# Kernel optimization log

Measured on AMD Instinct MI355X. Metric: run time of the kernel, lower is better.

## Reference

```python
import jax, jax.numpy as jnp
import numpy as np

TOP_K = 3
THRESH = 0.2
# scales=[1] -> multi_scale_fft reduces to one full-length window:
# combined_amplitudes = |rfft(x, axis=1)|.mean(channels)

def setup_inputs() -> dict:
    key = jax.random.key(0)
    x = jax.random.normal(key, (64, 4096, 64), dtype=jnp.float32)
    return {"x": x}

def _autocorr_score(xi, p):
    # xi: [T, C]; p: scalar int32 period (guaranteed in [2, T//2]).
    # Equivalent to mean over consecutive period-segments i of
    # cosine_similarity(flatten(seg_i), flatten(seg_{i+1})) — computed via
    # prefix sums of lag-p cross products so the segment reshape never needs
    # a data-dependent shape.
    T, C = xi.shape
    t = jnp.arange(T)
    tp = t + p
    m = (tp < T).astype(xi.dtype)
    xs = xi[jnp.clip(tp, 0, T - 1)]                  # [T, C] rows shifted by p
    r = (xi * xs).sum(-1) * m                        # <x[t], x[t+p]>
    q = (xi * xi).sum(-1)                            # ||x[t]||^2
    z = jnp.zeros((1,), xi.dtype)
    CR = jnp.concatenate([z, jnp.cumsum(r)])         # [T+1]
    CQ = jnp.concatenate([z, jnp.cumsum(q)])
    nper = T // p
    i = jnp.arange(T // 2)                           # max possible segments (p>=2)
    seg = i < (nper - 1)
    s = jnp.clip(i * p, 0, T)
    e = jnp.clip((i + 1) * p, 0, T)
    e2 = jnp.clip((i + 2) * p, 0, T)
    dots = CR[e] - CR[s]                             # flat dot(seg_i, seg_{i+1})
    na = jnp.sqrt(jnp.maximum(CQ[e] - CQ[s], 0.0))
    nb = jnp.sqrt(jnp.maximum(CQ[e2] - CQ[e], 0.0))
    cos = dots / jnp.maximum(na * nb, 1e-8)          # F.cosine_similarity eps
    denom = jnp.maximum(nper - 1, 1).astype(xi.dtype)
    score = jnp.where(seg, cos, 0.0).sum() / denom
    return jnp.where(nper >= 2, score, 0.0)

def reference(x):
    B, T, C = x.shape
    half = T // 2
    # multi-scale FFT with scales=[1]: single window == full sequence
    amps = jnp.abs(jnp.fft.rfft(x, axis=1)).mean(-1)       # [B, T//2+1]
    _, idx = jax.lax.top_k(amps, 2 * TOP_K)                 # [B, 2K]
    period_f = T / (idx + 1).astype(jnp.float32)            # candidate periods
    in_range = (period_f >= 2.0) & (period_f <= half)       # float-period filter
    p_int = jnp.clip(jnp.floor(period_f).astype(jnp.int32), 2, half)
    pf_floor = jnp.floor(period_f)
    in_range_int = (pf_floor >= 2.0) & (pf_floor <= half)   # int-period filter
    # autocorrelation validation score per (batch, candidate)
    scores = jax.vmap(lambda xi, ps: jax.vmap(lambda p: _autocorr_score(xi, p))(ps))(x, p_int)  # [B, 2K]
    valid = in_range & in_range_int & (scores > THRESH)
    # deterministic fallback periods (torch.randint branch unreachable for TOP_K=3)
    common = np.array([T // 4, T // 3, T // 2, int(T / 1.5)], dtype=np.int32)
    common = common[(common >= 2) & (common <= half)]
    add = jnp.asarray(common)                               # [>= TOP_K]

    def select(p_row, v_row):
        order = jnp.argsort(jnp.logical_not(v_row), stable=True)  # valid first, order kept
        sp = p_row[order][:TOP_K]
        cnt = jnp.minimum(v_row.sum(), TOP_K)
        j = jnp.arange(TOP_K)
        filled = jnp.where(j < cnt, sp, add[jnp.clip(j - cnt, 0, add.shape[0] - 1)])
        w = jnp.where(j < cnt, 1.0, 0.5)
        return filled.astype(jnp.float32), w.astype(jnp.float32)

    periods, weights = jax.vmap(select)(p_int, valid)       # [B, TOP_K] each
    return periods, weights
```

## Files before the change

kernel.cpp:

```cpp
#include <hip/hip_runtime.h>
#include <math.h>

#define T_LEN 4096
#define C_CH 64
#define B_N 64
#define NBINS 2049
#define K2 6
#define TOPK 3
#define THRESH_V 0.2f

#define PIDX(i) ((i) + ((i) >> 5))
#define ZSZ (T_LEN + (T_LEN >> 5))

__device__ __forceinline__ unsigned short f2bf(float v) {
    unsigned int u = __float_as_uint(v);
    u += 0x7FFFu + ((u >> 16) & 1u);
    return (unsigned short)(u >> 16);
}
__device__ __forceinline__ float bf2f(unsigned short h) {
    return __uint_as_float(((unsigned int)h) << 16);
}

__device__ __forceinline__ float2 cmul(float2 a, float2 b) {
    return make_float2(a.x * b.x - a.y * b.y, a.x * b.y + a.y * b.x);
}
__device__ __forceinline__ float2 cadd(float2 a, float2 b) { return make_float2(a.x + b.x, a.y + b.y); }
__device__ __forceinline__ float2 csub(float2 a, float2 b) { return make_float2(a.x - b.x, a.y - b.y); }

__device__ __forceinline__ void dft16(float2* v) {
    const float C2 = 0.70710678118654752f;
    const float C1 = 0.92387953251128676f;
    const float S1 = 0.38268343236508977f;
    const int br[16] = {0, 8, 4, 12, 2, 10, 6, 14, 1, 9, 5, 13, 3, 11, 7, 15};
    float2 a[16];
#pragma unroll
    for (int i = 0; i < 16; ++i) a[i] = v[br[i]];
#pragma unroll
    for (int g = 0; g < 16; g += 2) {
        float2 t = a[g + 1];
        a[g + 1] = csub(a[g], t);
        a[g] = cadd(a[g], t);
    }
#pragma unroll
    for (int g = 0; g < 16; g += 4) {
        {
            float2 t = a[g + 2];
            a[g + 2] = csub(a[g], t);
            a[g] = cadd(a[g], t);
        }
        {
            float2 t = make_float2(a[g + 3].y, -a[g + 3].x);
            a[g + 3] = csub(a[g + 1], t);
            a[g + 1] = cadd(a[g + 1], t);
        }
    }
    {
        const float2 W4[4] = {{1.f, 0.f}, {C2, -C2}, {0.f, -1.f}, {-C2, -C2}};
#pragma unroll
        for (int g = 0; g < 16; g += 8)
#pragma unroll
            for (int j = 0; j < 4; ++j) {
                float2 t = cmul(W4[j], a[g + 4 + j]);
                a[g + 4 + j] = csub(a[g + j], t);
                a[g + j] = cadd(a[g + j], t);
            }
    }
    {
        const float2 W8[8] = {{1.f, 0.f}, {C1, -S1}, {C2, -C2}, {S1, -C1},
                              {0.f, -1.f}, {-S1, -C1}, {-C2, -C2}, {-C1, -S1}};
#pragma unroll
        for (int j = 0; j < 8; ++j) {
            float2 t = cmul(W8[j], a[8 + j]);
            a[8 + j] = csub(a[j], t);
            a[j] = cadd(a[j], t);
        }
    }
#pragma unroll
    for (int i = 0; i < 16; ++i) v[i] = a[i];
}

__global__ void transpose_cvt_kernel(const float* __restrict__ x,
                                     unsigned short* __restrict__ xtbf) {
    __shared__ float tile[64][65];
    const int b = blockIdx.y;
    const int t0 = blockIdx.x * 64;
    const int lane = threadIdx.x & 63;
    const int w = threadIdx.x >> 6;
    const float* xb = x + (size_t)b * T_LEN * C_CH;
#pragma unroll
    for (int i = 0; i < 16; ++i) {
        int r = w * 16 + i;
        tile[r][lane] = xb[(size_t)(t0 + r) * C_CH + lane];
    }
    __syncthreads();
    const int half = lane >> 5;
    const int tc = (lane & 31) * 2;
#pragma unroll
    for (int it = 0; it < 8; ++it) {
        int c = it * 8 + w * 2 + half;
        float v0 = tile[tc][c];
        float v1 = tile[tc + 1][c];
        unsigned int o = (unsigned int)f2bf(v0) | ((unsigned int)f2bf(v1) << 16);
        unsigned int* dst = (unsigned int*)(xtbf + ((size_t)b * C_CH + c) * T_LEN + t0);
        dst[lane & 31] = o;
    }
}

template <int MODE>
__global__ void fft_amp_kernel(const void* __restrict__ srcv, float* __restrict__ amps) {
    __shared__ float2 Z[ZSZ];
    const int pair = blockIdx.x;
    const int b = blockIdx.y;
    const int tid = threadIdx.x;

    if (MODE == 0) {
        const unsigned short* r0 =
            (const unsigned short*)srcv + ((size_t)b * C_CH + pair * 2) * T_LEN;
        const unsigned short* r1 = r0 + T_LEN;
#pragma unroll
        for (int k = 0; k < 2; ++k) {
            int t0 = k * 2048 + tid * 8;
            uint4 u0 = *(const uint4*)(r0 + t0);
            uint4 u1 = *(const uint4*)(r1 + t0);
            unsigned int a[4] = {u0.x, u0.y, u0.z, u0.w};
            unsigned int c[4] = {u1.x, u1.y, u1.z, u1.w};
#pragma unroll
            for (int j = 0; j < 4; ++j) {
                Z[PIDX(t0 + 2 * j)] = make_float2(__uint_as_float(a[j] << 16),
                                                  __uint_as_float(c[j] << 16));
                Z[PIDX(t0 + 2 * j + 1)] = make_float2(__uint_as_float(a[j] & 0xFFFF0000u),
                                                      __uint_as_float(c[j] & 0xFFFF0000u));
            }
        }
    } else {
        const float* x = (const float*)srcv;
        const int c0 = pair * 2;
        for (int t = tid; t < T_LEN; t += 256)
            Z[PIDX(t)] = *(const float2*)(x + ((size_t)b * T_LEN + t) * C_CH + c0);
    }
    __syncthreads();

    {
        float2 v[16];
#pragma unroll
        for (int t = 0; t < 16; ++t) v[t] = Z[PIDX(tid + 256 * t)];
        dft16(v);
        float s, c;
        __sincosf(-(float)tid * 1.5339807878856412e-3f, &s, &c);
        float2 w1 = make_float2(c, s), w = w1;
#pragma unroll
        for (int r = 1; r < 16; ++r) {
            v[r] = cmul(v[r], w);
            w = cmul(w, w1);
        }
#pragma unroll
        for (int r = 0; r < 16; ++r) Z[PIDX(256 * r + tid)] = v[r];
    }
    __syncthreads();

    {
        const int r = tid >> 4, mu = tid & 15;
        float2 v[16];
#pragma unroll
        for (int nu = 0; nu < 16; ++nu) v[nu] = Z[PIDX(256 * r + mu + 16 * nu)];
        dft16(v);
        float s, c;
        __sincosf(-(float)mu * 2.4543692606170259e-2f, &s, &c);
        float2 w1 = make_float2(c, s), w = w1;
#pragma unroll
        for (int rho = 1; rho < 16; ++rho) {
            v[rho] = cmul(v[rho], w);
            w = cmul(w, w1);
        }
#pragma unroll
        for (int rho = 0; rho < 16; ++rho) Z[PIDX(256 * r + mu + 16 * rho)] = v[rho];
    }
    __builtin_amdgcn_wave_barrier();

    {
        const int r = tid >> 4, rho = tid & 15;
        float2 v[16];
#pragma unroll
        for (int mu = 0; mu < 16; ++mu) v[mu] = Z[PIDX(256 * r + mu + 16 * rho)];
        dft16(v);
#pragma unroll
        for (int mp = 0; mp < 16; ++mp) Z[PIDX(256 * r + mp + 16 * rho)] = v[mp];
    }
    __syncthreads();

    for (int k = tid; k < NBINS; k += 256) {
        int km = (T_LEN - k) & (T_LEN - 1);
        int sk = 256 * (k & 15) + 16 * ((k >> 4) & 15) + (k >> 8);
        int sm = 256 * (km & 15) + 16 * ((km >> 4) & 15) + (km >> 8);
        float2 zk = Z[PIDX(sk)];
        float2 zm = Z[PIDX(sm)];
        float ax = 0.5f * (zk.x + zm.x);
        float ay = 0.5f * (zk.y - zm.y);
        float bx = 0.5f * (zk.y + zm.y);
        float by = -0.5f * (zk.x - zm.x);
        float amp = sqrtf(ax * ax + ay * ay) + sqrtf(bx * bx + by * by);
        atomicAdd(&amps[(size_t)b * NBINS + k], amp);
    }
}

__global__ void topk_kernel(const float* __restrict__ amps, int* __restrict__ p_int,
                            int* __restrict__ preval) {
    __shared__ float vals[NBINS];
    __shared__ float sval[256];
    __shared__ int sidx[256];
    __shared__ int sel[K2];
    const int b = blockIdx.x;
    const int tid = threadIdx.x;
    for (int k = tid; k < NBINS; k += 256) vals[k] = amps[(size_t)b * NBINS + k];
    __syncthreads();
    for (int pass = 0; pass < K2; ++pass) {
        float bv = -INFINITY;
        int bi = NBINS;
        for (int k = tid; k < NBINS; k += 256) {
            float v = vals[k];
            if (v > bv || (v == bv && k < bi)) { bv = v; bi = k; }
        }
        sval[tid] = bv;
        sidx[tid] = bi;
        __syncthreads();
        for (int off = 128; off > 0; off >>= 1) {
            if (tid < off) {
                float ov = sval[tid + off];
                int oi = sidx[tid + off];
                if (ov > sval[tid] || (ov == sval[tid] && oi < sidx[tid])) {
                    sval[tid] = ov;
                    sidx[tid] = oi;
                }
            }
            __syncthreads();
        }
        if (tid == 0) {
            sel[pass] = sidx[0];
            vals[sidx[0]] = -INFINITY;
        }
        __syncthreads();
    }
    if (tid < K2) {
        int idx = sel[tid];
        float pf = (float)T_LEN / (float)(idx + 1);
        int ir = (pf >= 2.0f) && (pf <= (float)(T_LEN / 2));
        float pff = floorf(pf);
        int iri = (pff >= 2.0f) && (pff <= (float)(T_LEN / 2));
        int pi = (int)pff;
        pi = pi < 2 ? 2 : (pi > T_LEN / 2 ? T_LEN / 2 : pi);
        p_int[b * K2 + tid] = pi;
        preval[b * K2 + tid] = ir && iri;
    }
}

__global__ void rq_kernel(const unsigned short* __restrict__ xtbf,
                          const int* __restrict__ p_int, float* __restrict__ r_ws,
                          float* __restrict__ q_ws) {
    const int b = blockIdx.y;
    const int t = blockIdx.x * 64 + threadIdx.x;
    const unsigned short* xb = xtbf + (size_t)b * C_CH * T_LEN;

    int tpc[K2];
    float m[K2];
#pragma unroll
    for (int j = 0; j < K2; ++j) {
        int tp = t + p_int[b * K2 + j];
        m[j] = (tp < T_LEN) ? 1.f : 0.f;
        tpc[j] = (tp < T_LEN) ? tp : (T_LEN - 1);
    }

    float qacc = 0.f;
    float racc[K2] = {0.f, 0.f, 0.f, 0.f, 0.f, 0.f};
    for (int cc = 0; cc < C_CH; cc += 8) {
        float a[8];
        float bv[K2][8];
#pragma unroll
        for (int k = 0; k < 8; ++k) a[k] = bf2f(xb[(size_t)(cc + k) * T_LEN + t]);
#pragma unroll
        for (int j = 0; j < K2; ++j)
#pragma unroll
            for (int k = 0; k < 8; ++k)
                bv[j][k] = bf2f(xb[(size_t)(cc + k) * T_LEN + tpc[j]]);
#pragma unroll
        for (int k = 0; k < 8; ++k) {
            qacc += a[k] * a[k];
#pragma unroll
            for (int j = 0; j < K2; ++j) racc[j] += a[k] * bv[j][k];
        }
    }
    q_ws[(size_t)b * T_LEN + t] = qacc;
#pragma unroll
    for (int j = 0; j < K2; ++j)
        r_ws[((size_t)b * K2 + j) * T_LEN + t] = racc[j] * m[j];
}

__device__ __forceinline__ void block_scan_4096(float* a, float* tsum, int tid) {
    float loc[16];
    const int base = tid * 16;
    float s = 0.f;
#pragma unroll
    for (int i = 0; i < 16; ++i) {
        s += a[base + i];
        loc[i] = s;
    }
    tsum[tid] = s;
    __syncthreads();
    for (int off = 1; off < 256; off <<= 1) {
        float v = (tid >= off) ? tsum[tid - off] : 0.f;
        __syncthreads();
        tsum[tid] += v;
        __syncthreads();
    }
    float offs = tsum[tid] - s;
#pragma unroll
    for (int i = 0; i < 16; ++i) a[base + i] = offs + loc[i];
    __syncthreads();
}

__device__ __forceinline__ void do_select(int b, const int* p_int, const int* preval,
                                          const float* scores, float* out) {
    int sel[TOPK];
    int cnt = 0;
    for (int j = 0; j < K2; ++j) {
        if (preval[b * K2 + j] && scores[b * K2 + j] > THRESH_V) {
            if (cnt < TOPK) sel[cnt] = p_int[b * K2 + j];
            cnt++;
        }
    }
    if (cnt > TOPK) cnt = TOPK;
    int add[4];
    int nadd = 0;
    int cms[4] = {T_LEN / 4, T_LEN / 3, T_LEN / 2, (int)((float)T_LEN / 1.5f)};
    for (int i = 0; i < 4; ++i)
        if (cms[i] >= 2 && cms[i] <= T_LEN / 2) add[nadd++] = cms[i];
    for (int j = 0; j < TOPK; ++j) {
        float pv, wv;
        if (j < cnt) {
            pv = (float)sel[j];
            wv = 1.0f;
        } else {
            int a = j - cnt;
            if (a > nadd - 1) a = nadd - 1;
            pv = (float)add[a];
            wv = 0.5f;
        }
        out[b * TOPK + j] = pv;
        out[B_N * TOPK + b * TOPK + j] = wv;
    }
}

__global__ void score_kernel(const float* __restrict__ r_ws, const float* __restrict__ q_ws,
                             const int* __restrict__ p_int, const int* __restrict__ preval,
                             float* __restrict__ scores, int* __restrict__ counter,
                             float* __restrict__ out) {
    __shared__ float r_s[T_LEN];
    __shared__ float q_s[T_LEN];
    __shared__ float tsum[256];
    __shared__ int lastflag;
    const int cand = blockIdx.x;
    const int b = blockIdx.y;
    const int tid = threadIdx.x;
    const int p = p_int[b * K2 + cand];
    const float4* rsrc = (const float4*)(r_ws + ((size_t)b * K2 + cand) * T_LEN);
    const float4* qsrc = (const float4*)(q_ws + (size_t)b * T_LEN);
    for (int i = tid; i < T_LEN / 4; i += 256) {
        ((float4*)r_s)[i] = rsrc[i];
        ((float4*)q_s)[i] = qsrc[i];
    }
    __syncthreads();
    block_scan_4096(r_s, tsum, tid);
    block_scan_4096(q_s, tsum, tid);
    const int nper = T_LEN / p;
    float part = 0.f;
    for (int i = tid; i < nper - 1; i += 256) {
        int s0 = i * p;
        int e = s0 + p;
        int e2 = e + p;
        float crs = s0 ? r_s[s0 - 1] : 0.f;
        float dots = r_s[e - 1] - crs;
        float cqs = s0 ? q_s[s0 - 1] : 0.f;
        float qa = q_s[e - 1] - cqs;
        float qb = q_s[e2 - 1] - q_s[e - 1];
        float na = sqrtf(fmaxf(qa, 0.f));
        float nb = sqrtf(fmaxf(qb, 0.f));
        part += dots / fmaxf(na * nb, 1e-8f);
    }
    tsum[tid] = part;
    __syncthreads();
    for (int off = 128; off > 0; off >>= 1) {
        if (tid < off) tsum[tid] += tsum[tid + off];
        __syncthreads();
    }
    if (tid == 0) {
        scores[b * K2 + cand] = tsum[0] / (float)(nper - 1);
        __threadfence();
        int old = atomicAdd(counter, 1);
        lastflag = (old == K2 * B_N - 1) ? 1 : 0;
    }
    __syncthreads();
    if (lastflag && tid < B_N) {
        __threadfence();
        do_select(tid, p_int, preval, scores, out);
    }
}

__global__ void autocorr_kernel(const float* __restrict__ x, const int* __restrict__ p_int,
                                float* __restrict__ scores) {
    __shared__ float r_s[T_LEN];
    __shared__ float q_s[T_LEN];
    __shared__ float tsum[256];
    const int cand = blockIdx.x;
    const int b = blockIdx.y;
    const int tid = threadIdx.x;
    const int p = p_int[b * K2 + cand];
    const float* xb = x + (size_t)b * T_LEN * C_CH;
    for (int t = tid; t < T_LEN; t += 256) {
        const float4* row = (const float4*)(xb + (size_t)t * C_CH);
        float q = 0.f, r = 0.f;
        if (t + p < T_LEN) {
            const float4* row2 = (const float4*)(xb + (size_t)(t + p) * C_CH);
#pragma unroll
            for (int i = 0; i < 16; ++i) {
                float4 a = row[i], c = row2[i];
                r += a.x * c.x + a.y * c.y + a.z * c.z + a.w * c.w;
                q += a.x * a.x + a.y * a.y + a.z * a.z + a.w * a.w;
            }
        } else {
#pragma unroll
            for (int i = 0; i < 16; ++i) {
                float4 a = row[i];
                q += a.x * a.x + a.y * a.y + a.z * a.z + a.w * a.w;
            }
        }
        r_s[t] = r;
        q_s[t] = q;
    }
    __syncthreads();
    block_scan_4096(r_s, tsum, tid);
    block_scan_4096(q_s, tsum, tid);
    const int nper = T_LEN / p;
    float part = 0.f;
    for (int i = tid; i < nper - 1; i += 256) {
        int s0 = i * p;
        int e = s0 + p;
        int e2 = e + p;
        float crs = s0 ? r_s[s0 - 1] : 0.f;
        float dots = r_s[e - 1] - crs;
        float cqs = s0 ? q_s[s0 - 1] : 0.f;
        float qa = q_s[e - 1] - cqs;
        float qb = q_s[e2 - 1] - q_s[e - 1];
        float na = sqrtf(fmaxf(qa, 0.f));
        float nb = sqrtf(fmaxf(qb, 0.f));
        part += dots / fmaxf(na * nb, 1e-8f);
    }
    tsum[tid] = part;
    __syncthreads();
    for (int off = 128; off > 0; off >>= 1) {
        if (tid < off) tsum[tid] += tsum[tid + off];
        __syncthreads();
    }
    if (tid == 0) scores[b * K2 + cand] = tsum[0] / (float)(nper - 1);
}

__global__ void select_kernel(const int* __restrict__ p_int, const int* __restrict__ preval,
                              const float* __restrict__ scores, float* __restrict__ out) {
    const int b = threadIdx.x;
    if (b >= B_N) return;
    do_select(b, p_int, preval, scores, out);
}

static size_t align256(size_t v) { return (v + 255) & ~(size_t)255; }

extern "C" void kernel_launch(void* const* d_in, const int* in_sizes, int n_in,
                              void* d_out, int out_size, void* d_ws, size_t ws_size,
                              hipStream_t stream) {
    const float* x = (const float*)d_in[0];
    float* out = (float*)d_out;
    char* ws = (char*)d_ws;

    const size_t amps_b = align256((size_t)B_N * NBINS * sizeof(float));
    const size_t int_b = align256((size_t)B_N * K2 * sizeof(int));
    const size_t r_b = align256((size_t)B_N * K2 * T_LEN * sizeof(float));
    const size_t q_b = align256((size_t)B_N * T_LEN * sizeof(float));
    const size_t xtbf_b = align256((size_t)B_N * T_LEN * C_CH * sizeof(short));

    size_t off = 0;
    float* amps = (float*)(ws + off); off += amps_b;
    int* p_int = (int*)(ws + off); off += int_b;
    int* preval = (int*)(ws + off); off += int_b;
    float* scores = (float*)(ws + off); off += int_b;
    int* counter = (int*)(ws + off); off += 256;
    float* r_ws = (float*)(ws + off); off += r_b;
    float* q_ws = (float*)(ws + off); off += q_b;
    unsigned short* xtbf = (unsigned short*)(ws + off); off += xtbf_b;
    const size_t full_need = off;

    hipMemsetAsync(amps, 0, amps_b, stream);
    hipMemsetAsync(counter, 0, sizeof(int), stream);

    if (ws_size >= full_need) {
        transpose_cvt_kernel<<<dim3(T_LEN / 64, B_N), 256, 0, stream>>>(x, xtbf);
        fft_amp_kernel<0><<<dim3(C_CH / 2, B_N), 256, 0, stream>>>(xtbf, amps);
        topk_kernel<<<B_N, 256, 0, stream>>>(amps, p_int, preval);
        rq_kernel<<<dim3(T_LEN / 64, B_N), 64, 0, stream>>>(xtbf, p_int, r_ws, q_ws);
        score_kernel<<<dim3(K2, B_N), 256, 0, stream>>>(r_ws, q_ws, p_int, preval, scores,
                                                        counter, out);
    } else {
        fft_amp_kernel<1><<<dim3(C_CH / 2, B_N), 256, 0, stream>>>(x, amps);
        topk_kernel<<<B_N, 256, 0, stream>>>(amps, p_int, preval);
        autocorr_kernel<<<dim3(K2, B_N), 256, 0, stream>>>(x, p_int, scores);
        select_kernel<<<1, 64, 0, stream>>>(p_int, preval, scores, out);
    }
}
```

Before: 177.3 us.

## Fuse top-k into FFT kernel via last-block reduction, drop memsets and atomics

```diff
diff --git a/kernel.cpp b/kernel.cpp
--- a/kernel.cpp
+++ b/kernel.cpp
@@ -5,6 +5,7 @@
 #define C_CH 64
 #define B_N 64
 #define NBINS 2049
+#define APITCH 2052
 #define K2 6
 #define TOPK 3
 #define THRESH_V 0.2f
@@ -79,140 +80,8 @@
     for (int i = 0; i < 16; ++i) v[i] = a[i];
 }
 
-__global__ void transpose_cvt_kernel(const float* __restrict__ x,
-                                     unsigned short* __restrict__ xtbf) {
-    __shared__ float tile[64][65];
-    const int b = blockIdx.y;
-    const int t0 = blockIdx.x * 64;
-    const int lane = threadIdx.x & 63;
-    const int w = threadIdx.x >> 6;
-    const float* xb = x + (size_t)b * T_LEN * C_CH;
-#pragma unroll
-    for (int i = 0; i < 16; ++i) {
-        int r = w * 16 + i;
-        tile[r][lane] = xb[(size_t)(t0 + r) * C_CH + lane];
-    }
-    __syncthreads();
-    const int half = lane >> 5;
-    const int tc = (lane & 31) * 2;
-#pragma unroll
-    for (int it = 0; it < 8; ++it) {
-        int c = it * 8 + w * 2 + half;
-        float v0 = tile[tc][c];
-        float v1 = tile[tc + 1][c];
-        unsigned int o = (unsigned int)f2bf(v0) | ((unsigned int)f2bf(v1) << 16);
-        unsigned int* dst = (unsigned int*)(xtbf + ((size_t)b * C_CH + c) * T_LEN + t0);
-        dst[lane & 31] = o;
-    }
-}
-
-template <int MODE>
-__global__ void fft_amp_kernel(const void* __restrict__ srcv, float* __restrict__ amps) {
-    __shared__ float2 Z[ZSZ];
-    const int pair = blockIdx.x;
-    const int b = blockIdx.y;
-    const int tid = threadIdx.x;
-
-    if (MODE == 0) {
-        const unsigned short* r0 =
-            (const unsigned short*)srcv + ((size_t)b * C_CH + pair * 2) * T_LEN;
-        const unsigned short* r1 = r0 + T_LEN;
-#pragma unroll
-        for (int k = 0; k < 2; ++k) {
-            int t0 = k * 2048 + tid * 8;
-            uint4 u0 = *(const uint4*)(r0 + t0);
-            uint4 u1 = *(const uint4*)(r1 + t0);
-            unsigned int a[4] = {u0.x, u0.y, u0.z, u0.w};
-            unsigned int c[4] = {u1.x, u1.y, u1.z, u1.w};
-#pragma unroll
-            for (int j = 0; j < 4; ++j) {
-                Z[PIDX(t0 + 2 * j)] = make_float2(__uint_as_float(a[j] << 16),
-                                                  __uint_as_float(c[j] << 16));
-                Z[PIDX(t0 + 2 * j + 1)] = make_float2(__uint_as_float(a[j] & 0xFFFF0000u),
-                                                      __uint_as_float(c[j] & 0xFFFF0000u));
-            }
-        }
-    } else {
-        const float* x = (const float*)srcv;
-        const int c0 = pair * 2;
-        for (int t = tid; t < T_LEN; t += 256)
-            Z[PIDX(t)] = *(const float2*)(x + ((size_t)b * T_LEN + t) * C_CH + c0);
-    }
-    __syncthreads();
-
-    {
-        float2 v[16];
-#pragma unroll
-        for (int t = 0; t < 16; ++t) v[t] = Z[PIDX(tid + 256 * t)];
-        dft16(v);
-        float s, c;
-        __sincosf(-(float)tid * 1.5339807878856412e-3f, &s, &c);
-        float2 w1 = make_float2(c, s), w = w1;
-#pragma unroll
-        for (int r = 1; r < 16; ++r) {
-            v[r] = cmul(v[r], w);
-            w = cmul(w, w1);
-        }
-#pragma unroll
-        for (int r = 0; r < 16; ++r) Z[PIDX(256 * r + tid)] = v[r];
-    }
-    __syncthreads();
-
-    {
-        const int r = tid >> 4, mu = tid & 15;
-        float2 v[16];
-#pragma unroll
-        for (int nu = 0; nu < 16; ++nu) v[nu] = Z[PIDX(256 * r + mu + 16 * nu)];
-        dft16(v);
-        float s, c;
-        __sincosf(-(float)mu * 2.4543692606170259e-2f, &s, &c);
-        float2 w1 = make_float2(c, s), w = w1;
-#pragma unroll
-        for (int rho = 1; rho < 16; ++rho) {
-            v[rho] = cmul(v[rho], w);
-            w = cmul(w, w1);
-        }
-#pragma unroll
-        for (int rho = 0; rho < 16; ++rho) Z[PIDX(256 * r + mu + 16 * rho)] = v[rho];
-    }
-    __builtin_amdgcn_wave_barrier();
-
-    {
-        const int r = tid >> 4, rho = tid & 15;
-        float2 v[16];
-#pragma unroll
-        for (int mu = 0; mu < 16; ++mu) v[mu] = Z[PIDX(256 * r + mu + 16 * rho)];
-        dft16(v);
-#pragma unroll
-        for (int mp = 0; mp < 16; ++mp) Z[PIDX(256 * r + mp + 16 * rho)] = v[mp];
-    }
-    __syncthreads();
-
-    for (int k = tid; k < NBINS; k += 256) {
-        int km = (T_LEN - k) & (T_LEN - 1);
-        int sk = 256 * (k & 15) + 16 * ((k >> 4) & 15) + (k >> 8);
-        int sm = 256 * (km & 15) + 16 * ((km >> 4) & 15) + (km >> 8);
-        float2 zk = Z[PIDX(sk)];
-        float2 zm = Z[PIDX(sm)];
-        float ax = 0.5f * (zk.x + zm.x);
-        float ay = 0.5f * (zk.y - zm.y);
-        float bx = 0.5f * (zk.y + zm.y);
-        float by = -0.5f * (zk.x - zm.x);
-        float amp = sqrtf(ax * ax + ay * ay) + sqrtf(bx * bx + by * by);
-        atomicAdd(&amps[(size_t)b * NBINS + k], amp);
-    }
-}
-
-__global__ void topk_kernel(const float* __restrict__ amps, int* __restrict__ p_int,
-                            int* __restrict__ preval) {
-    __shared__ float vals[NBINS];
-    __shared__ float sval[256];
-    __shared__ int sidx[256];
-    __shared__ int sel[K2];
-    const int b = blockIdx.x;
-    const int tid = threadIdx.x;
-    for (int k = tid; k < NBINS; k += 256) vals[k] = amps[(size_t)b * NBINS + k];
-    __syncthreads();
+__device__ __forceinline__ void topk_select(float* vals, float* sval, int* sidx, int* sel,
+                                            int b, int tid, int* p_int, int* preval) {
     for (int pass = 0; pass < K2; ++pass) {
         float bv = -INFINITY;
         int bi = NBINS;
@@ -251,6 +120,174 @@
         p_int[b * K2 + tid] = pi;
         preval[b * K2 + tid] = ir && iri;
     }
+}
+
+__global__ void transpose_cvt_kernel(const float* __restrict__ x,
+                                     unsigned short* __restrict__ xtbf,
+                                     int* __restrict__ cnts) {
+    __shared__ float tile[64][65];
+    const int b = blockIdx.y;
+    const int t0 = blockIdx.x * 64;
+    const int lane = threadIdx.x & 63;
+    const int w = threadIdx.x >> 6;
+    if (blockIdx.x == 0 && blockIdx.y == 0 && threadIdx.x < B_N + 1)
+        cnts[threadIdx.x] = 0;
+    const float* xb = x + (size_t)b * T_LEN * C_CH;
+#pragma unroll
+    for (int i = 0; i < 16; ++i) {
+        int r = w * 16 + i;
+        tile[r][lane] = xb[(size_t)(t0 + r) * C_CH + lane];
+    }
+    __syncthreads();
+    const int half = lane >> 5;
+    const int tc = (lane & 31) * 2;
+#pragma unroll
+    for (int it = 0; it < 8; ++it) {
+        int c = it * 8 + w * 2 + half;
+        float v0 = tile[tc][c];
+        float v1 = tile[tc + 1][c];
+        unsigned int o = (unsigned int)f2bf(v0) | ((unsigned int)f2bf(v1) << 16);
+        unsigned int* dst = (unsigned int*)(xtbf + ((size_t)b * C_CH + c) * T_LEN + t0);
+        dst[lane & 31] = o;
+    }
+}
+
+template <int MODE>
+__global__ void fft_amp_kernel(const void* __restrict__ srcv, float* __restrict__ apart,
+                               int* __restrict__ cnts, int* __restrict__ p_int,
+                               int* __restrict__ preval) {
+    __shared__ float2 Z[ZSZ];
+    __shared__ int lastflag;
+    const int pair = blockIdx.x;
+    const int b = blockIdx.y;
+    const int tid = threadIdx.x;
+
+    if (MODE == 0) {
+        const unsigned short* r0 =
+            (const unsigned short*)srcv + ((size_t)b * C_CH + pair * 2) * T_LEN;
+        const unsigned short* r1 = r0 + T_LEN;
+#pragma unroll
+        for (int k = 0; k < 2; ++k) {
+            int t0 = k * 2048 + tid * 8;
+            uint4 u0 = *(const uint4*)(r0 + t0);
+            uint4 u1 = *(const uint4*)(r1 + t0);
+            unsigned int a[4] = {u0.x, u0.y, u0.z, u0.w};
+            unsigned int c[4] = {u1.x, u1.y, u1.z, u1.w};
+#pragma unroll
+            for (int j = 0; j < 4; ++j) {
+                Z[PIDX(t0 + 2 * j)] = make_float2(__uint_as_float(a[j] << 16),
+                                                  __uint_as_float(c[j] << 16));
+                Z[PIDX(t0 + 2 * j + 1)] = make_float2(__uint_as_float(a[j] & 0xFFFF0000u),
+                                                      __uint_as_float(c[j] & 0xFFFF0000u));
+            }
+        }
+    } else {
+        const float* x = (const float*)srcv;
+        const int c0 = pair * 2;
+        for (int t = tid; t < T_LEN; t += 256)
+            Z[PIDX(t)] = *(const float2*)(x + ((size_t)b * T_LEN + t) * C_CH + c0);
+    }
+    __syncthreads();
+
+    {
+        float2 v[16];
+#pragma unroll
+        for (int t = 0; t < 16; ++t) v[t] = Z[PIDX(tid + 256 * t)];
+        dft16(v);
+        float s, c;
+        __sincosf(-(float)tid * 1.5339807878856412e-3f, &s, &c);
+        float2 w1 = make_float2(c, s), w = w1;
+#pragma unroll
+        for (int r = 1; r < 16; ++r) {
+            v[r] = cmul(v[r], w);
+            w = cmul(w, w1);
+        }
+#pragma unroll
+        for (int r = 0; r < 16; ++r) Z[PIDX(256 * r + tid)] = v[r];
+    }
+    __syncthreads();
+
+    {
+        const int r = tid >> 4, mu = tid & 15;
+        float2 v[16];
+#pragma unroll
+        for (int nu = 0; nu < 16; ++nu) v[nu] = Z[PIDX(256 * r + mu + 16 * nu)];
+        dft16(v);
+        float s, c;
+        __sincosf(-(float)mu * 2.4543692606170259e-2f, &s, &c);
+        float2 w1 = make_float2(c, s), w = w1;
+#pragma unroll
+        for (int rho = 1; rho < 16; ++rho) {
+            v[rho] = cmul(v[rho], w);
+            w = cmul(w, w1);
+        }
+#pragma unroll
+        for (int rho = 0; rho < 16; ++rho) Z[PIDX(256 * r + mu + 16 * rho)] = v[rho];
+    }
+    __builtin_amdgcn_wave_barrier();
+
+    {
+        const int r = tid >> 4, rho = tid & 15;
+        float2 v[16];
+#pragma unroll
+        for (int mu = 0; mu < 16; ++mu) v[mu] = Z[PIDX(256 * r + mu + 16 * rho)];
+        dft16(v);
+#pragma unroll
+        for (int mp = 0; mp < 16; ++mp) Z[PIDX(256 * r + mp + 16 * rho)] = v[mp];
+    }
+    __syncthreads();
+
+    float* mypart = apart + ((size_t)b * 32 + pair) * APITCH;
+    for (int k = tid; k < NBINS; k += 256) {
+        int km = (T_LEN - k) & (T_LEN - 1);
+        int sk = 256 * (k & 15) + 16 * ((k >> 4) & 15) + (k >> 8);
+        int sm = 256 * (km & 15) + 16 * ((km >> 4) & 15) + (km >> 8);
+        float2 zk = Z[PIDX(sk)];
+        float2 zm = Z[PIDX(sm)];
+        float ax = 0.5f * (zk.x + zm.x);
+        float ay = 0.5f * (zk.y - zm.y);
+        float bx = 0.5f * (zk.y + zm.y);
+        float by = -0.5f * (zk.x - zm.x);
+        float amp = sqrtf(ax * ax + ay * ay) + sqrtf(bx * bx + by * by);
+        if (MODE == 0)
+            mypart[k] = amp;
+        else
+            atomicAdd(&apart[(size_t)b * NBINS + k], amp);
+    }
+
+    if (MODE != 0) return;
+
+    __threadfence();
+    if (tid == 0) lastflag = (atomicAdd(&cnts[b], 1) == 31) ? 1 : 0;
+    __syncthreads();
+    if (!lastflag) return;
+    __threadfence();
+
+    float* vals = (float*)Z;
+    float* sval = vals + NBINS;
+    int* sidx = (int*)(sval + 256);
+    int* sel = sidx + 256;
+    const float* bp = apart + (size_t)b * 32 * APITCH;
+    for (int k = tid; k < NBINS; k += 256) {
+        float s = 0.f;
+        for (int p2 = 0; p2 < 32; ++p2) s += bp[(size_t)p2 * APITCH + k];
+        vals[k] = s;
+    }
+    __syncthreads();
+    topk_select(vals, sval, sidx, sel, b, tid, p_int, preval);
+}
+
+__global__ void topk_kernel(const float* __restrict__ amps, int* __restrict__ p_int,
+                            int* __restrict__ preval) {
+    __shared__ float vals[NBINS];
+    __shared__ float sval[256];
+    __shared__ int sidx[256];
+    __shared__ int sel[K2];
+    const int b = blockIdx.x;
+    const int tid = threadIdx.x;
+    for (int k = tid; k < NBINS; k += 256) vals[k] = amps[(size_t)b * NBINS + k];
+    __syncthreads();
+    topk_select(vals, sval, sidx, sel, b, tid, p_int, preval);
 }
 
 __global__ void rq_kernel(const unsigned short* __restrict__ xtbf,
@@ -478,36 +515,34 @@
     float* out = (float*)d_out;
     char* ws = (char*)d_ws;
 
-    const size_t amps_b = align256((size_t)B_N * NBINS * sizeof(float));
+    const size_t cnt_b = 256;
     const size_t int_b = align256((size_t)B_N * K2 * sizeof(int));
+    const size_t apart_b = align256((size_t)B_N * 32 * APITCH * sizeof(float));
     const size_t r_b = align256((size_t)B_N * K2 * T_LEN * sizeof(float));
     const size_t q_b = align256((size_t)B_N * T_LEN * sizeof(float));
     const size_t xtbf_b = align256((size_t)B_N * T_LEN * C_CH * sizeof(short));
 
     size_t off = 0;
-    float* amps = (float*)(ws + off); off += amps_b;
+    int* cnts = (int*)(ws + off); off += cnt_b;
     int* p_int = (int*)(ws + off); off += int_b;
     int* preval = (int*)(ws + off); off += int_b;
     float* scores = (float*)(ws + off); off += int_b;
-    int* counter = (int*)(ws + off); off += 256;
+    float* apart = (float*)(ws + off); off += apart_b;
     float* r_ws = (float*)(ws + off); off += r_b;
     float* q_ws = (float*)(ws + off); off += q_b;
     unsigned short* xtbf = (unsigned short*)(ws + off); off += xtbf_b;
     const size_t full_need = off;
 
-    hipMemsetAsync(amps, 0, amps_b, stream);
-    hipMemsetAsync(counter, 0, sizeof(int), stream);
-
     if (ws_size >= full_need) {
-        transpose_cvt_kernel<<<dim3(T_LEN / 64, B_N), 256, 0, stream>>>(x, xtbf);
-        fft_amp_kernel<0><<<dim3(C_CH / 2, B_N), 256, 0, stream>>>(xtbf, amps);
-        topk_kernel<<<B_N, 256, 0, stream>>>(amps, p_int, preval);
+        transpose_cvt_kernel<<<dim3(T_LEN / 64, B_N), 256, 0, stream>>>(x, xtbf, cnts);
+        fft_amp_kernel<0><<<dim3(32, B_N), 256, 0, stream>>>(xtbf, apart, cnts, p_int, preval);
         rq_kernel<<<dim3(T_LEN / 64, B_N), 64, 0, stream>>>(xtbf, p_int, r_ws, q_ws);
         score_kernel<<<dim3(K2, B_N), 256, 0, stream>>>(r_ws, q_ws, p_int, preval, scores,
-                                                        counter, out);
+                                                        &cnts[B_N], out);
     } else {
-        fft_amp_kernel<1><<<dim3(C_CH / 2, B_N), 256, 0, stream>>>(x, amps);
-        topk_kernel<<<B_N, 256, 0, stream>>>(amps, p_int, preval);
+        hipMemsetAsync(apart, 0, (size_t)B_N * NBINS * sizeof(float), stream);
+        fft_amp_kernel<1><<<dim3(32, B_N), 256, 0, stream>>>(x, apart, cnts, p_int, preval);
+        topk_kernel<<<B_N, 256, 0, stream>>>(apart, p_int, preval);
         autocorr_kernel<<<dim3(K2, B_N), 256, 0, stream>>>(x, p_int, scores);
         select_kernel<<<1, 64, 0, stream>>>(p_int, preval, scores, out);
     }
```

Result: slower. 431.1 us (+143.1%).
